# Kernel optimization log

Hardware: AMD Instinct MI355X
Metric: run time of the kernel (lower is better)

Reference implementation:

```python
import jax, jax.numpy as jnp
import numpy as np

B, S, D, A = 32, 2048, 512, 256


def setup_inputs() -> dict:
    key = jax.random.key(0)
    ks = jax.random.split(key, 9)
    enc = jax.random.normal(ks[0], (B, S, D), dtype=jnp.float32)
    dec = jax.random.normal(ks[1], (B, 1, D), dtype=jnp.float32)
    prev = jax.random.uniform(ks[2], (B, S), dtype=jnp.float32)
    prev = prev / jnp.sum(prev, axis=1, keepdims=True)  # normalized prev attention
    noise = jax.random.normal(ks[3], (B, S), dtype=jnp.float32)
    W = jax.random.normal(ks[4], (A, D), dtype=jnp.float32) / np.sqrt(D)
    V = jax.random.normal(ks[5], (A, D), dtype=jnp.float32) / np.sqrt(D)
    b = jax.random.normal(ks[6], (A,), dtype=jnp.float32)
    v_w = jax.random.normal(ks[7], (1, A), dtype=jnp.float32)
    v_g = jnp.full((1,), np.sqrt(1.0 / A), dtype=jnp.float32)  # weight_norm g init
    v_bias = jax.random.normal(ks[8], (1,), dtype=jnp.float32)
    r = jnp.full((1,), -4.0, dtype=jnp.float32)
    return {"encoder_outputs": enc, "decoder_h": dec, "prev_alpha": prev,
            "noise": noise, "W": W, "V": V, "b": b, "v_w": v_w,
            "v_g": v_g, "v_bias": v_bias, "r": r}


def reference(encoder_outputs, decoder_h, prev_alpha, noise, W, V, b, v_w, v_g, v_bias, r):
    # Energy: tanh-MLP Bahdanau score with weight-normed output projection
    h = jnp.tanh(jnp.einsum('bsd,ad->bsa', encoder_outputs, W)
                 + jnp.einsum('bod,ad->boa', decoder_h, V)  # [B,1,A] broadcasts over S
                 + b)
    w_eff = v_g * v_w / jnp.linalg.norm(v_w)       # weight_norm: g * v / ||v||
    energy = jnp.einsum('bsa,oa->bso', h, w_eff)[..., 0] + v_bias[0] + r[0]  # [B,S]
    # Soft monotonic attention recurrence
    p_select = jax.nn.sigmoid(energy + noise)
    log1mp = jnp.log(jnp.clip(1.0 - p_select, 1e-10, 1.0))
    cumprod_1mp = jnp.exp(jnp.cumsum(log1mp, axis=1))  # safe_cumprod
    alpha = p_select * cumprod_1mp * jnp.cumsum(prev_alpha / cumprod_1mp, axis=1)
    # Context: enc^T @ alpha
    context = jnp.einsum('bsd,bs->bd', encoder_outputs, alpha)
    return context, alpha
```

## Files before the change

### kernel.cpp

```cpp
#include <hip/hip_runtime.h>
#include <math.h>

#define B_  32
#define S_  2048
#define D_  512
#define A_  256
#define BS_ (B_ * S_)

#define WEFF_OFF  0
#define DEC_OFF   256
#define EPART_OFF 8448
#define CTX_OFF   (8448 + BS_)

typedef _Float16 f16x8 __attribute__((ext_vector_type(8)));
typedef _Float16 half4 __attribute__((ext_vector_type(4)));
typedef float floatx4 __attribute__((ext_vector_type(4)));

__device__ __forceinline__ void glds16(const void* g, void* l) {
    __builtin_amdgcn_global_load_lds(
        (const __attribute__((address_space(1))) void*)g,
        (__attribute__((address_space(3))) void*)l, 16, 0, 0);
}

__global__ void ma_prep_kernel(const float* __restrict__ v_w,
                               const float* __restrict__ v_g,
                               const float* __restrict__ dec,
                               const float* __restrict__ V,
                               const float* __restrict__ bvec,
                               const float* __restrict__ W,
                               _Float16* __restrict__ W16,
                               float* __restrict__ ws) {
    __shared__ float sh[D_];
    const int bid = blockIdx.x, t = threadIdx.x;
    if (bid == 0) {
        float v = v_w[t];
        float sq = v * v;
        #pragma unroll
        for (int off = 32; off > 0; off >>= 1) sq += __shfl_down(sq, off, 64);
        if ((t & 63) == 0) sh[t >> 6] = sq;
        __syncthreads();
        float n2 = sh[0] + sh[1] + sh[2] + sh[3];
        ws[WEFF_OFF + t] = v_g[0] * v / sqrtf(n2);
    } else if (bid <= B_) {
        const int b = bid - 1;
        sh[t]       = dec[b * D_ + t];
        sh[t + 256] = dec[b * D_ + 256 + t];
        __syncthreads();
        const float4* Vr = (const float4*)(V + (size_t)t * D_);
        float acc = 0.f;
        #pragma unroll 4
        for (int k = 0; k < D_ / 4; ++k) {
            float4 v4 = Vr[k];
            acc = fmaf(v4.x, sh[4*k+0], acc);
            acc = fmaf(v4.y, sh[4*k+1], acc);
            acc = fmaf(v4.z, sh[4*k+2], acc);
            acc = fmaf(v4.w, sh[4*k+3], acc);
        }
        ws[DEC_OFF + b * A_ + t] = acc + bvec[t];
    } else {
        int i = (bid - (B_ + 1)) * 256 + t;
        float4 v = ((const float4*)W)[i];
        half4 h;
        h[0] = (_Float16)v.x; h[1] = (_Float16)v.y;
        h[2] = (_Float16)v.z; h[3] = (_Float16)v.w;
        ((half4*)W16)[i] = h;
    }
}

#define LDSTA 40
__global__ __launch_bounds__(512) void ma_energy_mfma(
        const float* __restrict__ enc,
        const _Float16* __restrict__ W16,
        const float* __restrict__ ws_in,
        float* __restrict__ energy) {
    __shared__ __align__(16) _Float16 As[2][128 * LDSTA];
    __shared__ __align__(16) _Float16 Bs[2][256 * 32];
    __shared__ float red[4][128];

    const int t  = threadIdx.x;
    const int bx = blockIdx.x;
    const size_t R0 = (size_t)bx * 128;
    const int batch = bx >> 4;

    const int lr = t >> 2;
    const int kc = (t & 3) * 8;
    const float* Ag = enc + (R0 + (size_t)lr) * D_ + kc;

    const int lane = t & 63, wid = t >> 6;
    const int wm = wid >> 2, wn = wid & 3;
    const int fr = lane & 15, kq = lane >> 4;

    const _Float16* Bg0 = W16 + (size_t)(wid * 32 + (lane >> 2)) * D_ + (lane & 3) * 8;
    const _Float16* Bg1 = Bg0 + (size_t)16 * D_;
    const int bdst0 = (wid * 32) * 32;
    const int bdst1 = (wid * 32 + 16) * 32;

    floatx4 acc[4][4];
    #pragma unroll
    for (int m = 0; m < 4; ++m)
        #pragma unroll
        for (int n = 0; n < 4; ++n) acc[m][n] = (floatx4)0.f;

    glds16(Bg0, &Bs[0][bdst0]);
    glds16(Bg1, &Bs[0][bdst1]);
    float4 a0 = *(const float4*)(Ag);
    float4 a1 = *(const float4*)(Ag + 4);
    {
        f16x8 h;
        h[0] = (_Float16)a0.x; h[1] = (_Float16)a0.y;
        h[2] = (_Float16)a0.z; h[3] = (_Float16)a0.w;
        h[4] = (_Float16)a1.x; h[5] = (_Float16)a1.y;
        h[6] = (_Float16)a1.z; h[7] = (_Float16)a1.w;
        *(f16x8*)&As[0][lr * LDSTA + kc] = h;
    }
    a0 = *(const float4*)(Ag + 32);
    a1 = *(const float4*)(Ag + 36);
    __syncthreads();

    for (int kt = 0; kt < 16; ++kt) {
        const int cur = kt & 1;
        if (kt < 15) {
            glds16(Bg0 + (kt + 1) * 32, &Bs[cur ^ 1][bdst0]);
            glds16(Bg1 + (kt + 1) * 32, &Bs[cur ^ 1][bdst1]);
        }
        f16x8 af[4], bf[4];
        #pragma unroll
        for (int m = 0; m < 4; ++m)
            af[m] = *(const f16x8*)&As[cur][(wm * 64 + m * 16 + fr) * LDSTA + kq * 8];
        #pragma unroll
        for (int n = 0; n < 4; ++n)
            bf[n] = *(const f16x8*)&Bs[cur][(wn * 64 + n * 16 + fr) * 32 + kq * 8];
        if (kt < 15) {
            f16x8 h;
            h[0] = (_Float16)a0.x; h[1] = (_Float16)a0.y;
            h[2] = (_Float16)a0.z; h[3] = (_Float16)a0.w;
            h[4] = (_Float16)a1.x; h[5] = (_Float16)a1.y;
            h[6] = (_Float16)a1.z; h[7] = (_Float16)a1.w;
            *(f16x8*)&As[cur ^ 1][lr * LDSTA + kc] = h;
        }
        if (kt < 14) {
            a0 = *(const float4*)(Ag + (kt + 2) * 32);
            a1 = *(const float4*)(Ag + (kt + 2) * 32 + 4);
        }
        #pragma unroll
        for (int m = 0; m < 4; ++m)
            #pragma unroll
            for (int n = 0; n < 4; ++n)
                acc[m][n] = __builtin_amdgcn_mfma_f32_16x16x32_f16(af[m], bf[n], acc[m][n], 0, 0, 0);
        __syncthreads();
    }

    const float* weff  = ws_in + WEFF_OFF;
    const float* dterm = ws_in + DEC_OFF + batch * A_;
    float wj[4], dj[4];
    #pragma unroll
    for (int n = 0; n < 4; ++n) {
        int a = wn * 64 + n * 16 + fr;
        wj[n] = weff[a];
        dj[n] = dterm[a];
    }
    #pragma unroll
    for (int m = 0; m < 4; ++m) {
        #pragma unroll
        for (int r = 0; r < 4; ++r) {
            float v = 0.f;
            #pragma unroll
            for (int n = 0; n < 4; ++n) {
                float x = acc[m][n][r] + dj[n];
                float e = __expf(2.f * x);
                v += (1.f - 2.f / (e + 1.f)) * wj[n];
            }
            #pragma unroll
            for (int mask = 1; mask < 16; mask <<= 1)
                v += __shfl_xor(v, mask, 64);
            if (fr == 0)
                red[wn][wm * 64 + m * 16 + (kq << 2) + r] = v;
        }
    }
    __syncthreads();
    if (t < 128)
        energy[R0 + t] = red[0][t] + red[1][t] + red[2][t] + red[3][t];
}

__global__ void ma_scan_kernel(const float* __restrict__ energy,
                               const float* __restrict__ noise,
                               const float* __restrict__ prev,
                               const float* __restrict__ v_bias,
                               const float* __restrict__ r,
                               float* __restrict__ alpha_out) {
    int b = blockIdx.x, t = threadIdx.x;
    const float bias = v_bias[0] + r[0];
    int base = b * S_ + t * 8;
    float p[8], av[8], bv[8];
    #pragma unroll
    for (int i = 0; i < 8; ++i) {
        float e = energy[base + i] + bias + noise[base + i];
        float pi = 1.f / (1.f + expf(-e));
        p[i]  = pi;
        av[i] = fmaxf(1.f - pi, 1e-10f);
        bv[i] = prev[base + i];
    }
    float Ai = 1.f, Bi = 0.f;
    #pragma unroll
    for (int i = 0; i < 8; ++i) { Bi = av[i] * Bi + bv[i]; Ai *= av[i]; }
    int lane = t & 63;
    #pragma unroll
    for (int off = 1; off < 64; off <<= 1) {
        float Ap = __shfl_up(Ai, off, 64);
        float Bp = __shfl_up(Bi, off, 64);
        if (lane >= off) { Bi = Ai * Bp + Bi; Ai = Ai * Ap; }
    }
    __shared__ float wA[4], wB[4];
    int w = t >> 6;
    if (lane == 63) { wA[w] = Ai; wB[w] = Bi; }
    __syncthreads();
    float Ax = __shfl_up(Ai, 1, 64);
    float Bx = __shfl_up(Bi, 1, 64);
    if (lane == 0) { Ax = 1.f; Bx = 0.f; }
    float PwA = 1.f, PwB = 0.f;
    for (int q = 0; q < w; ++q) { PwB = wA[q] * PwB + wB[q]; PwA *= wA[q]; }
    float T = Ax * PwB + Bx;
    #pragma unroll
    for (int i = 0; i < 8; ++i) {
        T = av[i] * T + bv[i];
        alpha_out[base + i] = p[i] * T;
    }
}

__global__ void ma_ctxpart_kernel(const float* __restrict__ enc,
                                  const float* __restrict__ alpha,
                                  float* __restrict__ cpart) {
    int b = blockIdx.x, sc = blockIdx.y, t = threadIdx.x;
    const float* e0 = enc + ((size_t)b * S_ + sc * 128) * D_;
    const float* al = alpha + b * S_ + sc * 128;
    float a0 = 0.f, a1 = 0.f;
    for (int s = 0; s < 128; ++s) {
        float avv = al[s];
        a0 = fmaf(e0[(size_t)s * D_ + t], avv, a0);
        a1 = fmaf(e0[(size_t)s * D_ + 256 + t], avv, a1);
    }
    cpart[((size_t)(sc * B_ + b)) * D_ + t]       = a0;
    cpart[((size_t)(sc * B_ + b)) * D_ + 256 + t] = a1;
}

__global__ void ma_ctxreduce_kernel(const float* __restrict__ cpart,
                                    float* __restrict__ ctx) {
    int b = blockIdx.x, t = threadIdx.x;
    #pragma unroll
    for (int h = 0; h < 2; ++h) {
        int d = t + h * 256;
        float s = 0.f;
        #pragma unroll
        for (int q = 0; q < 16; ++q) s += cpart[((size_t)(q * B_ + b)) * D_ + d];
        ctx[b * D_ + d] = s;
    }
}

extern "C" void kernel_launch(void* const* d_in, const int* in_sizes, int n_in,
                              void* d_out, int out_size, void* d_ws, size_t ws_size,
                              hipStream_t stream) {
    const float* enc    = (const float*)d_in[0];
    const float* dec    = (const float*)d_in[1];
    const float* prev   = (const float*)d_in[2];
    const float* noise  = (const float*)d_in[3];
    const float* W      = (const float*)d_in[4];
    const float* V      = (const float*)d_in[5];
    const float* bvec   = (const float*)d_in[6];
    const float* v_w    = (const float*)d_in[7];
    const float* v_g    = (const float*)d_in[8];
    const float* v_bias = (const float*)d_in[9];
    const float* r      = (const float*)d_in[10];

    float* out = (float*)d_out;
    float* ws  = (float*)d_ws;
    float* alpha = out + B_ * D_;
    _Float16* W16 = (_Float16*)(ws + CTX_OFF);

    ma_prep_kernel<<<1 + B_ + 128, 256, 0, stream>>>(v_w, v_g, dec, V, bvec, W, W16, ws);
    ma_energy_mfma<<<512, 512, 0, stream>>>(enc, W16, ws, ws + EPART_OFF);
    ma_scan_kernel<<<B_, 256, 0, stream>>>(ws + EPART_OFF, noise, prev, v_bias, r, alpha);
    dim3 gc(B_, 16);
    ma_ctxpart_kernel<<<gc, 256, 0, stream>>>(enc, alpha, ws + CTX_OFF);
    ma_ctxreduce_kernel<<<B_, 256, 0, stream>>>(ws + CTX_OFF, out);
}
```

Baseline: 85.94 us.

## Stream fp32 encoder tiles directly into swizzled LDS and split context reduction finer

The energy GEMM now loads fp32 encoder tiles straight into LDS with asynchronous global-to-LDS loads, replacing the old path that staged them through registers and converted to fp16 before storing. Both the A and B tiles use an XOR swizzle to avoid LDS bank conflicts, and the fp16 conversion happens at fragment-read time with packed round-toward-zero conversions. This removes the register round trip and gives more load overlap, at the cost of doubling A-tile LDS size and redoing the conversion per warp. Separately, the context partial kernel splits the sequence into 32 chunks instead of 16, giving more parallelism for the bandwidth-bound encoder re-read. The price is a larger partial buffer and more work in the final reduction.

```diff
diff --git a/kernel.cpp b/kernel.cpp
--- a/kernel.cpp
+++ b/kernel.cpp
@@ -13,6 +13,7 @@
 #define CTX_OFF   (8448 + BS_)
 
 typedef _Float16 f16x8 __attribute__((ext_vector_type(8)));
+typedef __fp16   fp16x2 __attribute__((ext_vector_type(2)));
 typedef _Float16 half4 __attribute__((ext_vector_type(4)));
 typedef float floatx4 __attribute__((ext_vector_type(4)));
 
@@ -67,13 +68,12 @@
     }
 }
 
-#define LDSTA 40
 __global__ __launch_bounds__(512) void ma_energy_mfma(
         const float* __restrict__ enc,
         const _Float16* __restrict__ W16,
         const float* __restrict__ ws_in,
         float* __restrict__ energy) {
-    __shared__ __align__(16) _Float16 As[2][128 * LDSTA];
+    __shared__ __align__(16) float    As[2][128 * 32];
     __shared__ __align__(16) _Float16 Bs[2][256 * 32];
     __shared__ float red[4][128];
 
@@ -82,18 +82,20 @@
     const size_t R0 = (size_t)bx * 128;
     const int batch = bx >> 4;
 
-    const int lr = t >> 2;
-    const int kc = (t & 3) * 8;
-    const float* Ag = enc + (R0 + (size_t)lr) * D_ + kc;
-
     const int lane = t & 63, wid = t >> 6;
     const int wm = wid >> 2, wn = wid & 3;
     const int fr = lane & 15, kq = lane >> 4;
 
-    const _Float16* Bg0 = W16 + (size_t)(wid * 32 + (lane >> 2)) * D_ + (lane & 3) * 8;
-    const _Float16* Bg1 = Bg0 + (size_t)16 * D_;
-    const int bdst0 = (wid * 32) * 32;
-    const int bdst1 = (wid * 32 + 16) * 32;
+    const int arow = t >> 3, ac = t & 7;
+    const float* AgS0 = enc + (R0 + (size_t)arow) * D_ + (ac ^ (arow & 7)) * 4;
+    const float* AgS1 = AgS0 + (size_t)64 * D_;
+    const int brow = t >> 2, bc = t & 3;
+    const _Float16* BgS0 = W16 + (size_t)brow * D_ + (bc ^ ((brow >> 1) & 3)) * 8;
+    const _Float16* BgS1 = BgS0 + (size_t)128 * D_;
+
+    const int axc0 = ((2 * kq)     ^ (fr & 7)) * 4;
+    const int axc1 = ((2 * kq + 1) ^ (fr & 7)) * 4;
+    const int bxo  = (kq ^ ((fr >> 1) & 3)) * 8;
 
     floatx4 acc[4][4];
     #pragma unroll
@@ -101,47 +103,40 @@
         #pragma unroll
         for (int n = 0; n < 4; ++n) acc[m][n] = (floatx4)0.f;
 
-    glds16(Bg0, &Bs[0][bdst0]);
-    glds16(Bg1, &Bs[0][bdst1]);
-    float4 a0 = *(const float4*)(Ag);
-    float4 a1 = *(const float4*)(Ag + 4);
-    {
-        f16x8 h;
-        h[0] = (_Float16)a0.x; h[1] = (_Float16)a0.y;
-        h[2] = (_Float16)a0.z; h[3] = (_Float16)a0.w;
-        h[4] = (_Float16)a1.x; h[5] = (_Float16)a1.y;
-        h[6] = (_Float16)a1.z; h[7] = (_Float16)a1.w;
-        *(f16x8*)&As[0][lr * LDSTA + kc] = h;
-    }
-    a0 = *(const float4*)(Ag + 32);
-    a1 = *(const float4*)(Ag + 36);
+    glds16(AgS0, &As[0][wid * 256]);
+    glds16(AgS1, &As[0][wid * 256 + 2048]);
+    glds16(BgS0, &Bs[0][wid * 512]);
+    glds16(BgS1, &Bs[0][wid * 512 + 4096]);
     __syncthreads();
 
+    #pragma unroll 1
     for (int kt = 0; kt < 16; ++kt) {
         const int cur = kt & 1;
         if (kt < 15) {
-            glds16(Bg0 + (kt + 1) * 32, &Bs[cur ^ 1][bdst0]);
-            glds16(Bg1 + (kt + 1) * 32, &Bs[cur ^ 1][bdst1]);
-        }
-        f16x8 af[4], bf[4];
-        #pragma unroll
-        for (int m = 0; m < 4; ++m)
-            af[m] = *(const f16x8*)&As[cur][(wm * 64 + m * 16 + fr) * LDSTA + kq * 8];
+            const int nxt = cur ^ 1;
+            const int ko = (kt + 1) * 32;
+            glds16(AgS0 + ko, &As[nxt][wid * 256]);
+            glds16(AgS1 + ko, &As[nxt][wid * 256 + 2048]);
+            glds16(BgS0 + ko, &Bs[nxt][wid * 512]);
+            glds16(BgS1 + ko, &Bs[nxt][wid * 512 + 4096]);
+        }
+        f16x8 af[4];
+        #pragma unroll
+        for (int m = 0; m < 4; ++m) {
+            const int rbase = (wm * 64 + m * 16 + fr) * 32;
+            float4 lo = *(const float4*)&As[cur][rbase + axc0];
+            float4 hi = *(const float4*)&As[cur][rbase + axc1];
+            union { fp16x2 h2[4]; f16x8 v; } u;
+            u.h2[0] = __builtin_amdgcn_cvt_pkrtz(lo.x, lo.y);
+            u.h2[1] = __builtin_amdgcn_cvt_pkrtz(lo.z, lo.w);
+            u.h2[2] = __builtin_amdgcn_cvt_pkrtz(hi.x, hi.y);
+            u.h2[3] = __builtin_amdgcn_cvt_pkrtz(hi.z, hi.w);
+            af[m] = u.v;
+        }
+        f16x8 bf[4];
         #pragma unroll
         for (int n = 0; n < 4; ++n)
-            bf[n] = *(const f16x8*)&Bs[cur][(wn * 64 + n * 16 + fr) * 32 + kq * 8];
-        if (kt < 15) {
-            f16x8 h;
-            h[0] = (_Float16)a0.x; h[1] = (_Float16)a0.y;
-            h[2] = (_Float16)a0.z; h[3] = (_Float16)a0.w;
-            h[4] = (_Float16)a1.x; h[5] = (_Float16)a1.y;
-            h[6] = (_Float16)a1.z; h[7] = (_Float16)a1.w;
-            *(f16x8*)&As[cur ^ 1][lr * LDSTA + kc] = h;
-        }
-        if (kt < 14) {
-            a0 = *(const float4*)(Ag + (kt + 2) * 32);
-            a1 = *(const float4*)(Ag + (kt + 2) * 32 + 4);
-        }
+            bf[n] = *(const f16x8*)&Bs[cur][(wn * 64 + n * 16 + fr) * 32 + bxo];
         #pragma unroll
         for (int m = 0; m < 4; ++m)
             #pragma unroll
@@ -231,10 +226,10 @@
                                   const float* __restrict__ alpha,
                                   float* __restrict__ cpart) {
     int b = blockIdx.x, sc = blockIdx.y, t = threadIdx.x;
-    const float* e0 = enc + ((size_t)b * S_ + sc * 128) * D_;
-    const float* al = alpha + b * S_ + sc * 128;
+    const float* e0 = enc + ((size_t)b * S_ + sc * 64) * D_;
+    const float* al = alpha + b * S_ + sc * 64;
     float a0 = 0.f, a1 = 0.f;
-    for (int s = 0; s < 128; ++s) {
+    for (int s = 0; s < 64; ++s) {
         float avv = al[s];
         a0 = fmaf(e0[(size_t)s * D_ + t], avv, a0);
         a1 = fmaf(e0[(size_t)s * D_ + 256 + t], avv, a1);
@@ -251,7 +246,7 @@
         int d = t + h * 256;
         float s = 0.f;
         #pragma unroll
-        for (int q = 0; q < 16; ++q) s += cpart[((size_t)(q * B_ + b)) * D_ + d];
+        for (int q = 0; q < 32; ++q) s += cpart[((size_t)(q * B_ + b)) * D_ + d];
         ctx[b * D_ + d] = s;
     }
 }
@@ -279,7 +274,7 @@
     ma_prep_kernel<<<1 + B_ + 128, 256, 0, stream>>>(v_w, v_g, dec, V, bvec, W, W16, ws);
     ma_energy_mfma<<<512, 512, 0, stream>>>(enc, W16, ws, ws + EPART_OFF);
     ma_scan_kernel<<<B_, 256, 0, stream>>>(ws + EPART_OFF, noise, prev, v_bias, r, alpha);
-    dim3 gc(B_, 16);
+    dim3 gc(B_, 32);
     ma_ctxpart_kernel<<<gc, 256, 0, stream>>>(enc, alpha, ws + CTX_OFF);
     ma_ctxreduce_kernel<<<B_, 256, 0, stream>>>(ws + CTX_OFF, out);
 }
```

Result: faster. 77.83 us (-9.4%).
